# Kernel tuning notes

Hardware: AMD Instinct MI355X
Metric: run time of the kernel (lower is better)

The kernel has to match this reference:

```python
import jax, jax.numpy as jnp
import numpy as np

B, T, S_ENC, H, V = 8, 128, 400, 256, 50257


def setup_inputs() -> dict:
    key = jax.random.key(0)
    ks = jax.random.split(key, 16)
    inp = {
        "input_tokens": jax.random.randint(ks[0], (B, S_ENC), 0, V),
        "context": jax.random.normal(ks[1], (B, T, H), dtype=jnp.float32),
        "decoder_input": jax.random.normal(ks[2], (B, T, H), dtype=jnp.float32),
        "decoder_output": jax.random.normal(ks[3], (B, T, H), dtype=jnp.float32),
        "vocab_dist": jax.random.uniform(ks[4], (B, T, V), dtype=jnp.float32),
        "attn_dist": jax.random.uniform(ks[5], (B, T, S_ENC), dtype=jnp.float32),
        "encoder_outputs": jax.random.normal(ks[6], (B, S_ENC, H), dtype=jnp.float32),
        # Linear(H, 1) params for the three p_gen projections
        "Wc": jax.random.normal(ks[7], (H, 1), dtype=jnp.float32) / np.sqrt(H),
        "bc": jnp.zeros((1,), dtype=jnp.float32),
        "Wo": jax.random.normal(ks[8], (H, 1), dtype=jnp.float32) / np.sqrt(H),
        "bo": jnp.zeros((1,), dtype=jnp.float32),
        "Wi": jax.random.normal(ks[9], (H, 1), dtype=jnp.float32) / np.sqrt(H),
        "bi": jnp.zeros((1,), dtype=jnp.float32),
    }
    return inp


def reference(input_tokens, context, decoder_input, decoder_output, vocab_dist,
              attn_dist, encoder_outputs, Wc, bc, Wo, bo, Wi, bi):
    # p_gen: sigmoid of sum of three Linear(H,1) projections -> [B, T, 1]
    p_gen = jax.nn.sigmoid(
        context @ Wc + bc + decoder_output @ Wo + bo + decoder_input @ Wi + bi
    )
    # copy distribution: scatter_add attn_dist into a [B, T, V] zeros tensor
    # along the vocab axis at the source token ids (broadcast over T).
    b_idx = jnp.arange(vocab_dist.shape[0])[:, None, None]   # [B,1,1]
    t_idx = jnp.arange(vocab_dist.shape[1])[None, :, None]   # [1,T,1]
    copy_dist = jnp.zeros_like(vocab_dist).at[
        b_idx, t_idx, input_tokens[:, None, :]
    ].add(attn_dist)
    # gated mix (same math as torch source: vocab_dist * p_gen + (1-p_gen) * log_softmax(copy))
    final_dist = vocab_dist * p_gen + (1.0 - p_gen) * jax.nn.log_softmax(copy_dist, axis=2)
    return final_dist
```

## Files before the change

kernel.cpp:

```cpp
#include <hip/hip_runtime.h>
#include <math.h>

#define B 8
#define T 128
#define S_ENC 400
#define H 256
#define V 50257
#define HASH_SZ 1024

typedef float vfloat4 __attribute__((ext_vector_type(4)));

__global__ __launch_bounds__(256) void prep_kernel(
    const int*   __restrict__ tokens,
    const float* __restrict__ context,
    const float* __restrict__ dec_in,
    const float* __restrict__ dec_out,
    const float* __restrict__ attn,
    const float* __restrict__ Wc, const float* __restrict__ bc,
    const float* __restrict__ Wo, const float* __restrict__ bo,
    const float* __restrict__ Wi, const float* __restrict__ bi,
    float4* __restrict__ params)
{
    __shared__ int   hkey[HASH_SZ];
    __shared__ float hval[HASH_SZ];
    __shared__ float s_pg[4];
    __shared__ float s_m[4];
    __shared__ int   s_n[4];
    __shared__ float s_se[4];
    __shared__ float s_mb;

    const int bt   = blockIdx.x;
    const int b    = bt >> 7;
    const int tid  = threadIdx.x;
    const int lane = tid & 63;
    const int wave = tid >> 6;

    #pragma unroll
    for (int i = tid; i < HASH_SZ; i += 256) {
        hkey[i] = -1;
        hval[i] = 0.0f;
    }
    __syncthreads();

    {
        float v = context[bt * H + tid] * Wc[tid]
                + dec_out[bt * H + tid] * Wo[tid]
                + dec_in [bt * H + tid] * Wi[tid];
        #pragma unroll
        for (int off = 32; off; off >>= 1) v += __shfl_down(v, off, 64);
        if (lane == 0) s_pg[wave] = v;
    }

    for (int s = tid; s < S_ENC; s += 256) {
        const int   tk = tokens[b * S_ENC + s];
        const float a  = attn[bt * S_ENC + s];
        unsigned h = ((unsigned)tk * 2654435761u >> 16) & (HASH_SZ - 1);
        for (;;) {
            int prev = atomicCAS(&hkey[h], -1, tk);
            if (prev == -1 || prev == tk) { atomicAdd(&hval[h], a); break; }
            h = (h + 1) & (HASH_SZ - 1);
        }
    }
    __syncthreads();

    {
        float m = 0.0f;
        int   n = 0;
        #pragma unroll
        for (int i = tid; i < HASH_SZ; i += 256) {
            if (hkey[i] != -1) { m = fmaxf(m, hval[i]); n++; }
        }
        #pragma unroll
        for (int off = 32; off; off >>= 1) {
            m  = fmaxf(m, __shfl_down(m, off, 64));
            n += __shfl_down(n, off, 64);
        }
        if (lane == 0) { s_m[wave] = m; s_n[wave] = n; }
    }
    __syncthreads();
    if (tid == 0) s_mb = fmaxf(fmaxf(s_m[0], s_m[1]), fmaxf(s_m[2], s_m[3]));
    __syncthreads();

    {
        const float m = s_mb;
        float se = 0.0f;
        #pragma unroll
        for (int i = tid; i < HASH_SZ; i += 256) {
            if (hkey[i] != -1) se += expf(hval[i] - m);
        }
        #pragma unroll
        for (int off = 32; off; off >>= 1) se += __shfl_down(se, off, 64);
        if (lane == 0) s_se[wave] = se;
    }
    __syncthreads();

    if (tid == 0) {
        const float m   = s_mb;
        const int   nnz = s_n[0] + s_n[1] + s_n[2] + s_n[3];
        float se  = s_se[0] + s_se[1] + s_se[2] + s_se[3]
                  + (float)(V - nnz) * expf(-m);
        float lse = m + logf(se);
        float x   = s_pg[0] + s_pg[1] + s_pg[2] + s_pg[3]
                  + bc[0] + bo[0] + bi[0];
        float p   = 1.0f / (1.0f + expf(-x));
        float q   = 1.0f - p;
        params[bt] = make_float4(p, q * lse, q, 0.0f);
    }
}

__global__ __launch_bounds__(256) void mix_kernel(
    const vfloat4* __restrict__ vocab,
    const float4*  __restrict__ params,
    vfloat4* __restrict__ out)
{
    const int idx = blockIdx.x * 256 + threadIdx.x;
    const int e   = idx * 4;
    const int bt  = e / V;
    const int rem = e - bt * V;

    vfloat4 v = __builtin_nontemporal_load(&vocab[idx]);
    vfloat4 o;
    if (rem + 4 <= V) {
        const float4 P = params[bt];
        o = v * P.x - P.y;
    } else {
        #pragma unroll
        for (int j = 0; j < 4; ++j) {
            int btj = (e + j) / V;
            float4 P = params[btj];
            o[j] = v[j] * P.x - P.y;
        }
    }
    __builtin_nontemporal_store(o, &out[idx]);
}

__global__ __launch_bounds__(256) void scatter_kernel(
    const int*   __restrict__ tokens,
    const float* __restrict__ attn,
    const float4* __restrict__ params,
    float* __restrict__ out)
{
    const int idx = blockIdx.x * 256 + threadIdx.x;
    const int bt  = idx / S_ENC;
    const int s   = idx - bt * S_ENC;
    const int b   = bt >> 7;
    const int tok = tokens[b * S_ENC + s];
    const float g = params[bt].z;
    atomicAdd(out + (size_t)bt * V + tok, g * attn[idx]);
}

extern "C" void kernel_launch(void* const* d_in, const int* in_sizes, int n_in,
                              void* d_out, int out_size, void* d_ws, size_t ws_size,
                              hipStream_t stream) {
    const int*   tokens  = (const int*)  d_in[0];
    const float* context = (const float*)d_in[1];
    const float* dec_in  = (const float*)d_in[2];
    const float* dec_out = (const float*)d_in[3];
    const float* vocab   = (const float*)d_in[4];
    const float* attn    = (const float*)d_in[5];
    const float* Wc = (const float*)d_in[7];
    const float* bc = (const float*)d_in[8];
    const float* Wo = (const float*)d_in[9];
    const float* bo = (const float*)d_in[10];
    const float* Wi = (const float*)d_in[11];
    const float* bi = (const float*)d_in[12];

    float*  out    = (float*) d_out;
    float4* params = (float4*)d_ws;

    prep_kernel<<<B * T, 256, 0, stream>>>(tokens, context, dec_in, dec_out,
                                           attn, Wc, bc, Wo, bo, Wi, bi, params);

    const int total4 = (B * T * V) / 4;
    mix_kernel<<<total4 / 256, 256, 0, stream>>>(
        (const vfloat4*)vocab, (const float4*)params, (vfloat4*)out);

    scatter_kernel<<<(B * T * S_ENC) / 256, 256, 0, stream>>>(
        tokens, attn, params, out);
}
```

Baseline: 407.8 us.

## Fuse copy-distribution scatter into mix kernel via per-batch unique-token tables

Adds a build kernel that deduplicates source tokens per batch into a unique list and a rank map. The prep kernel then accumulates attention per unique token into a compact array and writes scaled copy values. The mix kernel scans the unique tokens of its rows, stashes in shared memory those falling in its 1024-element window, and adds them in-register before the store. This removes the separate global-atomic scatter kernel, at the cost of every mix block rereading the per-row unique lists from cache and an extra launch.

```diff
diff --git a/kernel.cpp b/kernel.cpp
--- a/kernel.cpp
+++ b/kernel.cpp
@@ -10,8 +10,50 @@
 
 typedef float vfloat4 __attribute__((ext_vector_type(4)));
 
+
+__global__ __launch_bounds__(256) void build_kernel(
+    const int* __restrict__ tokens,
+    int* __restrict__ u, int* __restrict__ rnk, int* __restrict__ cnt)
+{
+    __shared__ int hk[HASH_SZ];
+    __shared__ int hr[HASH_SZ];
+    __shared__ int c;
+    const int b = blockIdx.x, tid = threadIdx.x;
+
+    for (int i = tid; i < HASH_SZ; i += 256) hk[i] = -1;
+    if (tid == 0) c = 0;
+    __syncthreads();
+
+    for (int s = tid; s < S_ENC; s += 256) {
+        const int tk = tokens[b * S_ENC + s];
+        unsigned h = ((unsigned)tk * 2654435761u >> 16) & (HASH_SZ - 1);
+        for (;;) {
+            int prev = atomicCAS(&hk[h], -1, tk);
+            if (prev == -1 || prev == tk) break;
+            h = (h + 1) & (HASH_SZ - 1);
+        }
+    }
+    __syncthreads();
+
+    for (int i = tid; i < HASH_SZ; i += 256) {
+        if (hk[i] != -1) {
+            const int r = atomicAdd(&c, 1);
+            hr[i] = r;
+            u[b * S_ENC + r] = hk[i];
+        }
+    }
+    __syncthreads();
+
+    for (int s = tid; s < S_ENC; s += 256) {
+        const int tk = tokens[b * S_ENC + s];
+        unsigned h = ((unsigned)tk * 2654435761u >> 16) & (HASH_SZ - 1);
+        while (hk[h] != tk) h = (h + 1) & (HASH_SZ - 1);
+        rnk[b * S_ENC + s] = hr[h];
+    }
+    if (tid == 0) cnt[b] = c;
+}
+
 __global__ __launch_bounds__(256) void prep_kernel(
-    const int*   __restrict__ tokens,
     const float* __restrict__ context,
     const float* __restrict__ dec_in,
     const float* __restrict__ dec_out,
@@ -19,28 +61,19 @@
     const float* __restrict__ Wc, const float* __restrict__ bc,
     const float* __restrict__ Wo, const float* __restrict__ bo,
     const float* __restrict__ Wi, const float* __restrict__ bi,
-    float4* __restrict__ params)
+    const int* __restrict__ rnk, const int* __restrict__ cnt,
+    float4* __restrict__ params, float* __restrict__ vs)
 {
-    __shared__ int   hkey[HASH_SZ];
-    __shared__ float hval[HASH_SZ];
-    __shared__ float s_pg[4];
-    __shared__ float s_m[4];
-    __shared__ int   s_n[4];
-    __shared__ float s_se[4];
-    __shared__ float s_mb;
-
+    __shared__ float val[S_ENC];
+    __shared__ float s_pg[4], s_m[4], s_se[4];
+    __shared__ float s_mb, s_q;
     const int bt   = blockIdx.x;
     const int b    = bt >> 7;
     const int tid  = threadIdx.x;
     const int lane = tid & 63;
     const int wave = tid >> 6;
 
-    #pragma unroll
-    for (int i = tid; i < HASH_SZ; i += 256) {
-        hkey[i] = -1;
-        hval[i] = 0.0f;
-    }
-    __syncthreads();
+    for (int i = tid; i < S_ENC; i += 256) val[i] = 0.0f;
 
     {
         float v = context[bt * H + tid] * Wc[tid]
@@ -50,103 +83,114 @@
         for (int off = 32; off; off >>= 1) v += __shfl_down(v, off, 64);
         if (lane == 0) s_pg[wave] = v;
     }
-
-    for (int s = tid; s < S_ENC; s += 256) {
-        const int   tk = tokens[b * S_ENC + s];
-        const float a  = attn[bt * S_ENC + s];
-        unsigned h = ((unsigned)tk * 2654435761u >> 16) & (HASH_SZ - 1);
-        for (;;) {
-            int prev = atomicCAS(&hkey[h], -1, tk);
-            if (prev == -1 || prev == tk) { atomicAdd(&hval[h], a); break; }
-            h = (h + 1) & (HASH_SZ - 1);
-        }
-    }
-    __syncthreads();
-
+    __syncthreads();
+
+    for (int s = tid; s < S_ENC; s += 256)
+        atomicAdd(&val[rnk[b * S_ENC + s]], attn[bt * S_ENC + s]);
+    __syncthreads();
+
+    const int n = cnt[b];
     {
         float m = 0.0f;
-        int   n = 0;
-        #pragma unroll
-        for (int i = tid; i < HASH_SZ; i += 256) {
-            if (hkey[i] != -1) { m = fmaxf(m, hval[i]); n++; }
-        }
-        #pragma unroll
-        for (int off = 32; off; off >>= 1) {
-            m  = fmaxf(m, __shfl_down(m, off, 64));
-            n += __shfl_down(n, off, 64);
-        }
-        if (lane == 0) { s_m[wave] = m; s_n[wave] = n; }
+        for (int i = tid; i < n; i += 256) m = fmaxf(m, val[i]);
+        #pragma unroll
+        for (int off = 32; off; off >>= 1) m = fmaxf(m, __shfl_down(m, off, 64));
+        if (lane == 0) s_m[wave] = m;
     }
     __syncthreads();
     if (tid == 0) s_mb = fmaxf(fmaxf(s_m[0], s_m[1]), fmaxf(s_m[2], s_m[3]));
     __syncthreads();
-
     {
         const float m = s_mb;
         float se = 0.0f;
-        #pragma unroll
-        for (int i = tid; i < HASH_SZ; i += 256) {
-            if (hkey[i] != -1) se += expf(hval[i] - m);
-        }
+        for (int i = tid; i < n; i += 256) se += expf(val[i] - m);
         #pragma unroll
         for (int off = 32; off; off >>= 1) se += __shfl_down(se, off, 64);
         if (lane == 0) s_se[wave] = se;
     }
     __syncthreads();
-
     if (tid == 0) {
         const float m   = s_mb;
-        const int   nnz = s_n[0] + s_n[1] + s_n[2] + s_n[3];
         float se  = s_se[0] + s_se[1] + s_se[2] + s_se[3]
-                  + (float)(V - nnz) * expf(-m);
+                  + (float)(V - n) * expf(-m);
         float lse = m + logf(se);
         float x   = s_pg[0] + s_pg[1] + s_pg[2] + s_pg[3]
                   + bc[0] + bo[0] + bi[0];
         float p   = 1.0f / (1.0f + expf(-x));
         float q   = 1.0f - p;
         params[bt] = make_float4(p, q * lse, q, 0.0f);
-    }
-}
+        s_q = q;
+    }
+    __syncthreads();
+    const float q = s_q;
+    for (int i = tid; i < n; i += 256) vs[bt * S_ENC + i] = q * val[i];
+}
+
+#define STASH_MAX 800
 
 __global__ __launch_bounds__(256) void mix_kernel(
     const vfloat4* __restrict__ vocab,
     const float4*  __restrict__ params,
+    const int*     __restrict__ u,
+    const int*     __restrict__ cnt,
+    const float*   __restrict__ vs,
     vfloat4* __restrict__ out)
 {
-    const int idx = blockIdx.x * 256 + threadIdx.x;
-    const int e   = idx * 4;
-    const int bt  = e / V;
-    const int rem = e - bt * V;
-
+    __shared__ int   s_d[STASH_MAX];
+    __shared__ float s_v[STASH_MAX];
+    __shared__ int   s_k;
+    const int tid = threadIdx.x;
+    const int idx = blockIdx.x * 256 + tid;
+    const int e0  = blockIdx.x << 10;
+    const int bt0 = e0 / V;
+    const int btL = (e0 + 1023) / V;
+
+    if (tid == 0) s_k = 0;
     vfloat4 v = __builtin_nontemporal_load(&vocab[idx]);
+    __syncthreads();
+
+    for (int r = bt0; r <= btL; ++r) {
+        const int base = r * V;
+        const int bb   = r >> 7;
+        const int n    = cnt[bb];
+        const int*   ub = u  + bb * S_ENC;
+        const float* vb = vs + r  * S_ENC;
+        for (int i = tid; i < n; i += 256) {
+            const int d = base + ub[i] - e0;
+            if ((unsigned)d < 1024u) {
+                const int slot = atomicAdd(&s_k, 1);
+                s_d[slot] = d;
+                s_v[slot] = vb[i];
+            }
+        }
+    }
+    __syncthreads();
+
     vfloat4 o;
-    if (rem + 4 <= V) {
-        const float4 P = params[bt];
+    const int eb = idx << 2;
+    if (bt0 == btL) {
+        const float4 P = params[bt0];
         o = v * P.x - P.y;
     } else {
         #pragma unroll
         for (int j = 0; j < 4; ++j) {
-            int btj = (e + j) / V;
-            float4 P = params[btj];
+            const int bt = (eb + j) / V;
+            const float4 P = params[bt];
             o[j] = v[j] * P.x - P.y;
         }
     }
+
+    const int k  = s_k;
+    const int my = eb - e0;
+    for (int j = 0; j < k; ++j) {
+        const int   d = s_d[j] - my;
+        const float a = s_v[j];
+        o[0] += (d == 0) ? a : 0.0f;
+        o[1] += (d == 1) ? a : 0.0f;
+        o[2] += (d == 2) ? a : 0.0f;
+        o[3] += (d == 3) ? a : 0.0f;
+    }
     __builtin_nontemporal_store(o, &out[idx]);
-}
-
-__global__ __launch_bounds__(256) void scatter_kernel(
-    const int*   __restrict__ tokens,
-    const float* __restrict__ attn,
-    const float4* __restrict__ params,
-    float* __restrict__ out)
-{
-    const int idx = blockIdx.x * 256 + threadIdx.x;
-    const int bt  = idx / S_ENC;
-    const int s   = idx - bt * S_ENC;
-    const int b   = bt >> 7;
-    const int tok = tokens[b * S_ENC + s];
-    const float g = params[bt].z;
-    atomicAdd(out + (size_t)bt * V + tok, g * attn[idx]);
 }
 
 extern "C" void kernel_launch(void* const* d_in, const int* in_sizes, int n_in,
@@ -165,16 +209,21 @@
     const float* Wi = (const float*)d_in[11];
     const float* bi = (const float*)d_in[12];
 
-    float*  out    = (float*) d_out;
-    float4* params = (float4*)d_ws;
-
-    prep_kernel<<<B * T, 256, 0, stream>>>(tokens, context, dec_in, dec_out,
-                                           attn, Wc, bc, Wo, bo, Wi, bi, params);
+    float* out = (float*)d_out;
+    char*  ws  = (char*)d_ws;
+    float4* params = (float4*)ws;
+    int*    u      = (int*)  (ws + 16384);
+    int*    rnk    = (int*)  (ws + 29184);
+    int*    cnt    = (int*)  (ws + 41984);
+    float*  vs     = (float*)(ws + 42048);
+
+    build_kernel<<<B, 256, 0, stream>>>(tokens, u, rnk, cnt);
+
+    prep_kernel<<<B * T, 256, 0, stream>>>(context, dec_in, dec_out, attn,
+                                           Wc, bc, Wo, bo, Wi, bi,
+                                           rnk, cnt, params, vs);
 
     const int total4 = (B * T * V) / 4;
     mix_kernel<<<total4 / 256, 256, 0, stream>>>(
-        (const vfloat4*)vocab, (const float4*)params, (vfloat4*)out);
-
-    scatter_kernel<<<(B * T * S_ENC) / 256, 256, 0, stream>>>(
-        tokens, attn, params, out);
-}
+        (const vfloat4*)vocab, (const float4*)params, u, cnt, vs, (vfloat4*)out);
+}
```

After: 389.9 us. 4.4% less time.
